# Performance work log

Hardware: AMD Instinct MI355X
Metric: run time of the kernel (lower is better)

## Reference

```python
import jax, jax.numpy as jnp
import numpy as np

B, L, E = 16, 1022, 1280
D, H, FF, NL = 512, 8, 2048, 4
DH = D // H
EPS = 1e-5


def layer_norm(x, s, b):
    m = jnp.mean(x, axis=-1, keepdims=True)
    v = jnp.mean(jnp.square(x - m), axis=-1, keepdims=True)
    return (x - m) * jax.lax.rsqrt(v + EPS) * s + b


def setup_inputs() -> dict:
    key = jax.random.key(0)
    ks = jax.random.split(key, 12)
    s = 0.02
    return {
        "embeddings": jax.random.normal(ks[0], (B, L, E), jnp.float32),
        "mask": jnp.ones((B, L), jnp.float32),
        "position": jnp.tile(jnp.arange(L, dtype=jnp.int32)[None, :], (B, 1)),
        "proj_w": jax.random.normal(ks[1], (D, E), jnp.float32) * s,
        "proj_b": jnp.zeros((D,), jnp.float32),
        "proj_ln_s": jnp.ones((D,), jnp.float32),
        "proj_ln_b": jnp.zeros((D,), jnp.float32),
        "ln1_s": jnp.ones((NL, D), jnp.float32),
        "ln1_b": jnp.zeros((NL, D), jnp.float32),
        "in_w": jax.random.normal(ks[2], (NL, 3 * D, D), jnp.float32) * s,
        "in_b": jnp.zeros((NL, 3 * D), jnp.float32),
        "out_w": jax.random.normal(ks[3], (NL, D, D), jnp.float32) * s,
        "out_b": jnp.zeros((NL, D), jnp.float32),
        "ln2_s": jnp.ones((NL, D), jnp.float32),
        "ln2_b": jnp.zeros((NL, D), jnp.float32),
        "w1": jax.random.normal(ks[4], (NL, FF, D), jnp.float32) * s,
        "b1": jnp.zeros((NL, FF), jnp.float32),
        "w2": jax.random.normal(ks[5], (NL, D, FF), jnp.float32) * s,
        "b2": jnp.zeros((NL, D), jnp.float32),
        "h1_w": jax.random.normal(ks[6], (128, 2 * D), jnp.float32) * s,
        "h1_b": jnp.zeros((128,), jnp.float32),
        "hln_s": jnp.ones((128,), jnp.float32),
        "hln_b": jnp.zeros((128,), jnp.float32),
        "h2_w": jax.random.normal(ks[7], (1, 128), jnp.float32) * s,
        "h2_b": jnp.zeros((1,), jnp.float32),
    }


def _rope_tables():
    inv_freq = 1.0 / (10000.0 ** (jnp.arange(0, DH, 2, dtype=jnp.float32) / DH))
    t = jnp.arange(L, dtype=jnp.float32)
    freqs = jnp.outer(t, inv_freq)          # [L, DH/2]
    emb = jnp.concatenate([freqs, freqs], axis=-1)  # [L, DH]
    return jnp.cos(emb), jnp.sin(emb)


def _rotate_half(x):
    x1, x2 = jnp.split(x, 2, axis=-1)
    return jnp.concatenate([-x2, x1], axis=-1)


def _apply_rope(x, cos, sin):
    # x: [B, L, D] -> per-head rotation -> [B, L, D]
    xh = x.reshape(B, L, H, DH)
    xh = xh * cos[None, :, None, :] + _rotate_half(xh) * sin[None, :, None, :]
    return xh.reshape(B, L, D)


def _forward(embeddings, mask, proj_w, proj_b, proj_ln_s, proj_ln_b,
             ln1_s, ln1_b, in_w, in_b, out_w, out_b, ln2_s, ln2_b,
             w1, b1, w2, b2, h1_w, h1_b, hln_s, hln_b, h2_w, h2_b):
    cos, sin = _rope_tables()
    x = layer_norm(embeddings @ proj_w.T + proj_b, proj_ln_s, proj_ln_b)  # [B,L,D]
    pad = mask <= 0  # True where padded (~mask.bool())
    scale = 1.0 / jnp.sqrt(jnp.float32(DH))
    for i in range(NL):
        n = layer_norm(x, ln1_s[i], ln1_b[i])
        q_in = _apply_rope(n, cos, sin)
        k_in = _apply_rope(n, cos, sin)
        v_in = n
        wq, wk, wv = jnp.split(in_w[i], 3, axis=0)
        bq, bk, bv = jnp.split(in_b[i], 3, axis=0)
        qh = (q_in @ wq.T + bq).reshape(B, L, H, DH)
        kh = (k_in @ wk.T + bk).reshape(B, L, H, DH)
        vh = (v_in @ wv.T + bv).reshape(B, L, H, DH)
        scores = jnp.einsum('blhd,bmhd->bhlm', qh, kh) * scale
        scores = jnp.where(pad[:, None, None, :], jnp.float32(-1e9), scores)
        attn = jax.nn.softmax(scores, axis=-1)
        o = jnp.einsum('bhlm,bmhd->blhd', attn, vh).reshape(B, L, D)
        x = x + (o @ out_w[i].T + out_b[i])
        n2 = layer_norm(x, ln2_s[i], ln2_b[i])
        x = x + (jax.nn.relu(n2 @ w1[i].T + b1[i]) @ w2[i].T + b2[i])
    # masked mean pool
    gctx = (x * mask[..., None]).sum(axis=1) / mask.sum(axis=1, keepdims=True)  # [B,D]
    combined = jnp.concatenate([x, jnp.broadcast_to(gctx[:, None, :], (B, L, D))], axis=-1)
    h = jax.nn.relu(layer_norm(combined @ h1_w.T + h1_b, hln_s, hln_b))
    logits = (h @ h2_w.T + h2_b).squeeze(-1)  # [B,L]
    return logits


def reference(embeddings, mask, position, proj_w, proj_b, proj_ln_s, proj_ln_b,
              ln1_s, ln1_b, in_w, in_b, out_w, out_b, ln2_s, ln2_b,
              w1, b1, w2, b2, h1_w, h1_b, hln_s, hln_b, h2_w, h2_b):
    # position is accepted for API parity but unused (as in the torch module)
    return _forward(embeddings, mask, proj_w, proj_b, proj_ln_s, proj_ln_b,
                    ln1_s, ln1_b, in_w, in_b, out_w, out_b, ln2_s, ln2_b,
                    w1, b1, w2, b2, h1_w, h1_b, hln_s, hln_b, h2_w, h2_b)
```

## Files before the change

### kernel.cpp

```cpp
#include <hip/hip_runtime.h>
#include <cstdint>
#include <cstddef>

#define B_   16
#define L_   1022
#define E_   1280
#define D_   512
#define H_   8
#define FF_  2048
#define NL_  4
#define DH_  64
#define BL_  (B_*L_)
#define EPS_ 1e-5f
#define QSC_ 0.18033688011112042f

typedef unsigned short u16;
typedef unsigned int   u32;
typedef unsigned long long u64;
typedef float f32x4 __attribute__((ext_vector_type(4)));
typedef short s16x8 __attribute__((ext_vector_type(8)));
typedef u32 u32x4 __attribute__((ext_vector_type(4)));

__device__ __forceinline__ u16 f2bf(float f) {
    u32 u = __builtin_bit_cast(u32, f);
    u += 0x7fffu + ((u >> 16) & 1u);
    return (u16)(u >> 16);
}
__device__ __forceinline__ float bf2f(u16 u) {
    return __builtin_bit_cast(float, (u32)u << 16);
}
__device__ __forceinline__ u32 pack2bf(float a, float b) {
    return (u32)f2bf(a) | ((u32)f2bf(b) << 16);
}

__global__ __launch_bounds__(256)
void cast_k(const float* __restrict__ src, u16* __restrict__ dst, int n8) {
    int t = blockIdx.x * 256 + threadIdx.x;
    if (t >= n8) return;
    const float* s = src + (size_t)t * 8;
    float4 a = *(const float4*)(s);
    float4 b = *(const float4*)(s + 4);
    s16x8 o;
    o[0] = (short)f2bf(a.x); o[1] = (short)f2bf(a.y);
    o[2] = (short)f2bf(a.z); o[3] = (short)f2bf(a.w);
    o[4] = (short)f2bf(b.x); o[5] = (short)f2bf(b.y);
    o[6] = (short)f2bf(b.z); o[7] = (short)f2bf(b.w);
    *(s16x8*)(dst + (size_t)t * 8) = o;
}

__global__ __launch_bounds__(256)
void castq_k(const float* __restrict__ src, u16* __restrict__ dst, int n8) {
    int t = blockIdx.x * 256 + threadIdx.x;
    if (t >= n8) return;
    int row = t >> 6;
    float sc = (row % 1536) < 512 ? QSC_ : 1.0f;
    const float* s = src + (size_t)t * 8;
    float4 a = *(const float4*)(s);
    float4 b = *(const float4*)(s + 4);
    s16x8 o;
    o[0] = (short)f2bf(a.x * sc); o[1] = (short)f2bf(a.y * sc);
    o[2] = (short)f2bf(a.z * sc); o[3] = (short)f2bf(a.w * sc);
    o[4] = (short)f2bf(b.x * sc); o[5] = (short)f2bf(b.y * sc);
    o[6] = (short)f2bf(b.z * sc); o[7] = (short)f2bf(b.w * sc);
    *(s16x8*)(dst + (size_t)t * 8) = o;
}

__global__ __launch_bounds__(256)
void qbias_k(const float* __restrict__ ib, float* __restrict__ qbs) {
    int t = blockIdx.x * 256 + threadIdx.x;
    if (t >= NL_ * 1024) return;
    int i = t >> 10, j = t & 1023;
    float sc = j < 512 ? QSC_ : 1.0f;
    qbs[t] = ib[i * 1536 + j] * sc;
}

__global__ __launch_bounds__(256)
void h1cast_k(const float* __restrict__ src, u16* __restrict__ dst) {
    int t = blockIdx.x * 256 + threadIdx.x;
    if (t >= 128 * 512 / 8) return;
    int row = t >> 6, c8 = (t & 63) << 3;
    const float* s = src + (size_t)row * 1024 + c8;
    float4 a = *(const float4*)(s);
    float4 b = *(const float4*)(s + 4);
    s16x8 o;
    o[0] = (short)f2bf(a.x); o[1] = (short)f2bf(a.y);
    o[2] = (short)f2bf(a.z); o[3] = (short)f2bf(a.w);
    o[4] = (short)f2bf(b.x); o[5] = (short)f2bf(b.y);
    o[6] = (short)f2bf(b.z); o[7] = (short)f2bf(b.w);
    *(s16x8*)(dst + (size_t)row * 512 + c8) = o;
}

__global__ void tables_k(float* __restrict__ ct, float* __restrict__ st) {
    int idx = blockIdx.x * blockDim.x + threadIdx.x;
    if (idx >= L_ * DH_) return;
    int l = idx / DH_;
    int d = idx % DH_;
    int j = d & 31;
    float invf = powf(10000.0f, -(float)(2 * j) / (float)DH_);
    float ang = (float)l * invf;
    ct[idx] = cosf(ang);
    st[idx] = sinf(ang);
}

template<bool RELU, bool RESID, bool OUTBF, bool ROWBIAS>
__global__ __launch_bounds__(256)
void mgemm_k(const u16* __restrict__ A, const u16* __restrict__ W,
             const float* __restrict__ bias, const float* __restrict__ resid,
             void* __restrict__ Cout, int M, int N, int K)
{
    constexpr int LDT = 72;
    __shared__ u16 As[128 * LDT];
    __shared__ u16 Ws[128 * LDT];
    const int nt = N >> 7;
    const int bx = blockIdx.x % nt;
    const int by = blockIdx.x / nt;
    const int m0 = by << 7, n0 = bx << 7;
    const int tid = threadIdx.x;
    const int lane = tid & 63, wid = tid >> 6;
    const int wr = wid >> 1, wc = wid & 1;
    const int lr = lane & 15, lk = lane >> 4;

    f32x4 acc[4][4];
#pragma unroll
    for (int m = 0; m < 4; m++)
#pragma unroll
        for (int n = 0; n < 4; n++) acc[m][n] = (f32x4)0.0f;

    for (int k0 = 0; k0 < K; k0 += 64) {
        s16x8 va[4], vw[4];
#pragma unroll
        for (int u = 0; u < 4; u++) {
            int ch = tid + (u << 8);
            int r = ch >> 3, c8 = (ch & 7) << 3;
            int ar = m0 + r; if (ar >= M) ar = M - 1;
            va[u] = *(const s16x8*)(A + (size_t)ar * K + k0 + c8);
            vw[u] = *(const s16x8*)(W + (size_t)(n0 + r) * K + k0 + c8);
        }
        __syncthreads();
#pragma unroll
        for (int u = 0; u < 4; u++) {
            int ch = tid + (u << 8);
            int r = ch >> 3, c8 = (ch & 7) << 3;
            *(s16x8*)&As[r * LDT + c8] = va[u];
            *(s16x8*)&Ws[r * LDT + c8] = vw[u];
        }
        __syncthreads();
#pragma unroll
        for (int kk = 0; kk < 2; kk++) {
            s16x8 af[4], bf[4];
#pragma unroll
            for (int m = 0; m < 4; m++)
                af[m] = *(const s16x8*)&As[(wr * 64 + m * 16 + lr) * LDT + kk * 32 + lk * 8];
#pragma unroll
            for (int n = 0; n < 4; n++)
                bf[n] = *(const s16x8*)&Ws[(wc * 64 + n * 16 + lr) * LDT + kk * 32 + lk * 8];
#pragma unroll
            for (int m = 0; m < 4; m++)
#pragma unroll
                for (int n = 0; n < 4; n++)
                    acc[m][n] = __builtin_amdgcn_mfma_f32_16x16x32_bf16(
                        af[m], bf[n], acc[m][n], 0, 0, 0);
        }
    }

    float bv[4];
    if constexpr (!ROWBIAS) {
#pragma unroll
        for (int n = 0; n < 4; n++) bv[n] = bias[n0 + wc * 64 + n * 16 + lr];
    }
#pragma unroll
    for (int m = 0; m < 4; m++) {
#pragma unroll
        for (int j = 0; j < 4; j++) {
            int row = m0 + wr * 64 + m * 16 + lk * 4 + j;
            if (row >= M) continue;
            const float* rb = nullptr;
            if constexpr (ROWBIAS) rb = bias + (size_t)(row / L_) * N;
#pragma unroll
            for (int n = 0; n < 4; n++) {
                int col = n0 + wc * 64 + n * 16 + lr;
                float c = acc[m][n][j];
                if constexpr (ROWBIAS) c += rb[col];
                else                   c += bv[n];
                if constexpr (RELU) c = fmaxf(c, 0.0f);
                if constexpr (RESID) c += resid[(size_t)row * N + col];
                if constexpr (OUTBF) ((u16*)Cout)[(size_t)row * N + col] = f2bf(c);
                else                 ((float*)Cout)[(size_t)row * N + col] = c;
            }
        }
    }
}

template<int DD, bool RELU, bool OUTBF>
__global__ __launch_bounds__(256)
void ln_k(const float* __restrict__ x, const float* __restrict__ s,
          const float* __restrict__ bb, void* __restrict__ out, int M)
{
    const int lane = threadIdx.x & 63;
    const int row = (blockIdx.x << 2) + (threadIdx.x >> 6);
    if (row >= M) return;
    const float* xr = x + (size_t)row * DD;
    constexpr int NV = DD / 64;
    float v[NV];
    if constexpr (NV == 8) {
        *(float4*)(v)     = *(const float4*)(xr + lane * 8);
        *(float4*)(v + 4) = *(const float4*)(xr + lane * 8 + 4);
    } else {
        float2 t = *(const float2*)(xr + lane * 2);
        v[0] = t.x; v[1] = t.y;
    }
    float sum = 0.f, sq = 0.f;
#pragma unroll
    for (int e = 0; e < NV; e++) { sum += v[e]; sq += v[e] * v[e]; }
#pragma unroll
    for (int msk = 1; msk < 64; msk <<= 1) {
        sum += __shfl_xor(sum, msk);
        sq  += __shfl_xor(sq, msk);
    }
    const float mean = sum * (1.0f / DD);
    const float var  = sq * (1.0f / DD) - mean * mean;
    const float rstd = rsqrtf(var + EPS_);
#pragma unroll
    for (int e = 0; e < NV; e++) {
        int d = lane * NV + e;
        float r = (v[e] - mean) * rstd * s[d] + bb[d];
        if constexpr (RELU) r = fmaxf(r, 0.0f);
        v[e] = r;
    }
    if constexpr (OUTBF) {
        u16* orow = (u16*)out + (size_t)row * DD;
        if constexpr (NV == 8) {
            s16x8 o;
#pragma unroll
            for (int e = 0; e < 8; e++) o[e] = (short)f2bf(v[e]);
            *(s16x8*)(orow + lane * 8) = o;
        } else {
            orow[lane * 2] = f2bf(v[0]); orow[lane * 2 + 1] = f2bf(v[1]);
        }
    } else {
        float* orow = (float*)out + (size_t)row * DD;
        if constexpr (NV == 8) {
            *(float4*)(orow + lane * 8)     = *(float4*)(v);
            *(float4*)(orow + lane * 8 + 4) = *(float4*)(v + 4);
        } else {
            float2 t; t.x = v[0]; t.y = v[1];
            *(float2*)(orow + lane * 2) = t;
        }
    }
}

__global__ __launch_bounds__(256)
void rope_k(const u16* __restrict__ n, const float* __restrict__ ct,
            const float* __restrict__ st, u16* __restrict__ r)
{
    int t = blockIdx.x * 256 + threadIdx.x;
    if (t >= BL_ * D_ / 8) return;
    int idx = t << 3;
    int l = (idx / D_) % L_;
    int d = idx & (D_ - 1);
    int dd = d & 63;
    s16x8 xv = *(const s16x8*)(n + idx);
    int pidx; float sgn;
    if (dd < 32) { pidx = idx + 32; sgn = -1.0f; }
    else         { pidx = idx - 32; sgn =  1.0f; }
    s16x8 pv = *(const s16x8*)(n + pidx);
    float4 c0 = *(const float4*)(ct + l * DH_ + dd);
    float4 c1 = *(const float4*)(ct + l * DH_ + dd + 4);
    float4 s0 = *(const float4*)(st + l * DH_ + dd);
    float4 s1 = *(const float4*)(st + l * DH_ + dd + 4);
    float cc[8] = {c0.x,c0.y,c0.z,c0.w,c1.x,c1.y,c1.z,c1.w};
    float ss[8] = {s0.x,s0.y,s0.z,s0.w,s1.x,s1.y,s1.z,s1.w};
    s16x8 o;
#pragma unroll
    for (int e = 0; e < 8; e++) {
        float xf = bf2f((u16)xv[e]);
        float pf = bf2f((u16)pv[e]);
        o[e] = (short)f2bf(xf * cc[e] + sgn * pf * ss[e]);
    }
    *(s16x8*)(r + idx) = o;
}

__global__ __launch_bounds__(256)
void attn_k(const u16* __restrict__ qk, const u16* __restrict__ v,
            const float* __restrict__ mask, u16* __restrict__ o)
{
    constexpr int LDA = 68;
    constexpr int TSZ = 64 * LDA;
    __shared__ u16 Kt[2 * TSZ];
    __shared__ u16 Vt[2 * TSZ];
    const int bh = blockIdx.x >> 4, qt = blockIdx.x & 15;
    const int b = bh >> 3, h = bh & 7;
    const int tid = threadIdx.x;
    const int lane = tid & 63, w = tid >> 6;
    const int lr = lane & 15, lg = lane >> 4;
    const size_t basebl = (size_t)b * L_;

    const int qrow = qt * 64 + w * 16 + lr;
    const int qc = qrow < L_ ? qrow : L_ - 1;
    s16x8 bq[2];
#pragma unroll
    for (int kk = 0; kk < 2; kk++)
        bq[kk] = *(const s16x8*)(qk + (basebl + qc) * 1024 + h * DH_ + kk * 32 + lg * 8);

    f32x4 oacc[4];
#pragma unroll
    for (int n = 0; n < 4; n++) oacc[n] = (f32x4)0.0f;
    float m_run = -1e30f, l_run = 0.f;

    const int st_key = tid >> 3;
    const int st_d8 = (tid & 7) << 3;
    const int src0 = lr + ((lane & 16) << 1);
    const int src1 = src0 + 16;
    const bool ahi = (lg >> 1) != 0;

    auto stage = [&](int buf, int kt_) {
#pragma unroll
        for (int u = 0; u < 2; u++) {
            int key = st_key + u * 32;
            int gk = kt_ * 64 + key; if (gk >= L_) gk = L_ - 1;
            s16x8 kv = *(const s16x8*)(qk + (basebl + gk) * 1024 + 512 + h * DH_ + st_d8);
            s16x8 vv = *(const s16x8*)(v  + (basebl + gk) * D_ + h * DH_ + st_d8);
            *(s16x8*)&Kt[buf * TSZ + key * LDA + st_d8] = kv;
#pragma unroll
            for (int e = 0; e < 8; e++)
                Vt[buf * TSZ + (st_d8 + e) * LDA + key] = (u16)vv[e];
        }
    };

    stage(0, 0);
    __syncthreads();

    for (int kt = 0; kt < 16; kt++) {
        const int cur = kt & 1;
        if (kt < 15) stage(cur ^ 1, kt + 1);

        int gkey = kt * 64 + lane;
        bool vb = (gkey < L_) && (mask[basebl + gkey] > 0.0f);
        u64 vm = __ballot(vb);

        f32x4 sacc[4];
#pragma unroll
        for (int n = 0; n < 4; n++) {
            sacc[n] = (f32x4)0.0f;
#pragma unroll
            for (int kk = 0; kk < 2; kk++) {
                s16x8 ak = *(const s16x8*)&Kt[cur * TSZ + (n * 16 + lr) * LDA + kk * 32 + lg * 8];
                sacc[n] = __builtin_amdgcn_mfma_f32_16x16x32_bf16(ak, bq[kk], sacc[n], 0, 0, 0);
            }
        }

        float p[4][4];
        float tm = -1e30f;
#pragma unroll
        for (int n = 0; n < 4; n++)
#pragma unroll
            for (int j = 0; j < 4; j++) {
                int kl = 16 * n + 4 * lg + j;
                float s = ((vm >> kl) & 1ull) ? sacc[n][j] : -1e30f;
                p[n][j] = s;
                tm = fmaxf(tm, s);
            }
        tm = fmaxf(tm, __shfl_xor(tm, 16));
        tm = fmaxf(tm, __shfl_xor(tm, 32));
        if (!__all(tm - m_run <= 8.0f)) {
            float nm = fmaxf(m_run, tm);
            float corr = exp2f(m_run - nm);
            l_run *= corr;
#pragma unroll
            for (int n = 0; n < 4; n++) oacc[n] *= corr;
            m_run = nm;
        }
        float ts = 0.f;
#pragma unroll
        for (int n = 0; n < 4; n++)
#pragma unroll
            for (int j = 0; j < 4; j++) {
                p[n][j] = exp2f(p[n][j] - m_run);
                ts += p[n][j];
            }
        ts += __shfl_xor(ts, 16);
        ts += __shfl_xor(ts, 32);
        l_run += ts;

        u32 pk[4][2];
#pragma unroll
        for (int n = 0; n < 4; n++) {
            pk[n][0] = pack2bf(p[n][0], p[n][1]);
            pk[n][1] = pack2bf(p[n][2], p[n][3]);
        }
        u32 r0[4][2], r1[4][2];
#pragma unroll
        for (int n = 0; n < 4; n++)
#pragma unroll
            for (int i = 0; i < 2; i++) {
                r0[n][i] = (u32)__shfl((int)pk[n][i], src0);
                r1[n][i] = (u32)__shfl((int)pk[n][i], src1);
            }
#pragma unroll
        for (int kk = 0; kk < 2; kk++) {
            u32x4 bw;
            bw[0] = ahi ? r0[2 * kk + 1][0] : r0[2 * kk][0];
            bw[1] = ahi ? r0[2 * kk + 1][1] : r0[2 * kk][1];
            bw[2] = ahi ? r1[2 * kk + 1][0] : r1[2 * kk][0];
            bw[3] = ahi ? r1[2 * kk + 1][1] : r1[2 * kk][1];
            s16x8 bp = __builtin_bit_cast(s16x8, bw);
#pragma unroll
            for (int n2 = 0; n2 < 4; n2++) {
                s16x8 av = *(const s16x8*)&Vt[cur * TSZ + (n2 * 16 + lr) * LDA + kk * 32 + lg * 8];
                oacc[n2] = __builtin_amdgcn_mfma_f32_16x16x32_bf16(av, bp, oacc[n2], 0, 0, 0);
            }
        }
        __syncthreads();
    }

    u16* Ol = &Kt[w * 16 * LDA];
    float inv = 1.0f / l_run;
#pragma unroll
    for (int n = 0; n < 4; n++)
#pragma unroll
        for (int j = 0; j < 4; j++)
            Ol[lr * LDA + 16 * n + 4 * lg + j] = f2bf(oacc[n][j] * inv);
    int orow = lane >> 2, oc = (lane & 3) * 16;
    int qg = qt * 64 + w * 16 + orow;
    if (qg < L_) {
        s16x8 o0 = *(const s16x8*)&Ol[orow * LDA + oc];
        s16x8 o1 = *(const s16x8*)&Ol[orow * LDA + oc + 8];
        *(s16x8*)(o + (basebl + qg) * D_ + h * DH_ + oc) = o0;
        *(s16x8*)(o + (basebl + qg) * D_ + h * DH_ + oc + 8) = o1;
    }
}

__global__ __launch_bounds__(512)
void pool1_k(const float* __restrict__ x, const float* __restrict__ mask,
             float* __restrict__ pp, float* __restrict__ mp)
{
    const int b = blockIdx.x, sp = blockIdx.y;
    const int d = threadIdx.x;
    const int l0 = sp * 64;
    float acc = 0.f;
    for (int l = l0; l < l0 + 64 && l < L_; l++)
        acc += x[((size_t)b * L_ + l) * D_ + d] * mask[b * L_ + l];
    pp[((size_t)b * 16 + sp) * D_ + d] = acc;
    if (d == 0) {
        float ms = 0.f;
        for (int l = l0; l < l0 + 64 && l < L_; l++) ms += mask[b * L_ + l];
        mp[b * 16 + sp] = ms;
    }
}

__global__ __launch_bounds__(512)
void pool2_k(const float* __restrict__ pp, const float* __restrict__ mp,
             float* __restrict__ g)
{
    const int b = blockIdx.x;
    const int d = threadIdx.x;
    float acc = 0.f, ms = 0.f;
#pragma unroll
    for (int sp = 0; sp < 16; sp++) {
        acc += pp[((size_t)b * 16 + sp) * D_ + d];
        ms += mp[b * 16 + sp];
    }
    g[b * D_ + d] = acc / ms;
}

__global__ __launch_bounds__(256)
void gpart_k(const float* __restrict__ g, const float* __restrict__ h1w,
             const float* __restrict__ h1b, float* __restrict__ gp)
{
    const int lane = threadIdx.x & 63;
    const int gid = (blockIdx.x << 2) + (threadIdx.x >> 6);
    const int b = gid >> 7, j = gid & 127;
    const float* wr = h1w + (size_t)j * (2 * D_) + D_;
    const float* gr = g + b * D_;
    float4 a0 = *(const float4*)(gr + lane * 8);
    float4 a1 = *(const float4*)(gr + lane * 8 + 4);
    float4 w0 = *(const float4*)(wr + lane * 8);
    float4 w1v = *(const float4*)(wr + lane * 8 + 4);
    float acc = a0.x * w0.x + a0.y * w0.y + a0.z * w0.z + a0.w * w0.w
              + a1.x * w1v.x + a1.y * w1v.y + a1.z * w1v.z + a1.w * w1v.w;
#pragma unroll
    for (int msk = 1; msk < 64; msk <<= 1) acc += __shfl_xor(acc, msk);
    if (lane == 0) gp[b * 128 + j] = acc + h1b[j];
}

__global__ __launch_bounds__(256)
void logits_k(const float* __restrict__ h, const float* __restrict__ w,
              const float* __restrict__ bsc, float* __restrict__ out, int M)
{
    const int lane = threadIdx.x & 63;
    const int row = (blockIdx.x << 2) + (threadIdx.x >> 6);
    if (row >= M) return;
    float2 hv = *(const float2*)(h + (size_t)row * 128 + lane * 2);
    float2 wv = *(const float2*)(w + lane * 2);
    float acc = hv.x * wv.x + hv.y * wv.y;
#pragma unroll
    for (int msk = 1; msk < 64; msk <<= 1) acc += __shfl_xor(acc, msk);
    if (lane == 0) out[row] = acc + bsc[0];
}

extern "C" void kernel_launch(void* const* d_in, const int* in_sizes, int n_in,
                              void* d_out, int out_size, void* d_ws, size_t ws_size,
                              hipStream_t stream)
{
    const float* emb       = (const float*)d_in[0];
    const float* mask      = (const float*)d_in[1];
    const float* proj_w    = (const float*)d_in[3];
    const float* proj_b    = (const float*)d_in[4];
    const float* proj_ln_s = (const float*)d_in[5];
    const float* proj_ln_b = (const float*)d_in[6];
    const float* ln1_s     = (const float*)d_in[7];
    const float* ln1_b     = (const float*)d_in[8];
    const float* in_w      = (const float*)d_in[9];
    const float* in_b      = (const float*)d_in[10];
    const float* out_w     = (const float*)d_in[11];
    const float* out_b     = (const float*)d_in[12];
    const float* ln2_s     = (const float*)d_in[13];
    const float* ln2_b     = (const float*)d_in[14];
    const float* w1        = (const float*)d_in[15];
    const float* b1        = (const float*)d_in[16];
    const float* w2        = (const float*)d_in[17];
    const float* b2        = (const float*)d_in[18];
    const float* h1_w      = (const float*)d_in[19];
    const float* h1_b      = (const float*)d_in[20];
    const float* hln_s     = (const float*)d_in[21];
    const float* hln_b     = (const float*)d_in[22];
    const float* h2_w      = (const float*)d_in[23];
    const float* h2_b      = (const float*)d_in[24];
    float* out = (float*)d_out;

    float* ws = (float*)d_ws;
    const size_t S = (size_t)BL_ * D_;
    float* X  = ws;
    float* Rf = ws + S;
    u16* QKB   = (u16*)(ws + S);
    u16* VB    = (u16*)(ws + 2 * S);
    u16* NbB   = (u16*)(ws + 2 * S) + S;
    u16* FFb16 = (u16*)(ws + 3 * S);
    u16* RopeB = FFb16;
    u16* embB  = FFb16;
    u16* RB    = (u16*)(ws + 4 * S);
    u16* projwB = (u16*)(ws + 5 * S);
    u16* iwB  = projwB + 512 * 1280;
    u16* owB  = iwB + (size_t)NL_ * 3 * D_ * D_;
    u16* w1B  = owB + (size_t)NL_ * D_ * D_;
    u16* w2B  = w1B + (size_t)NL_ * FF_ * D_;
    u16* h1wB = w2B + (size_t)NL_ * D_ * FF_;
    float* CT = ws + 5 * S + 6651904;
    float* ST = CT + L_ * DH_;
    float* GC = ST + L_ * DH_;
    float* GP = GC + B_ * D_;
    float* Pp = GP + B_ * 128;
    float* Mp = Pp + (size_t)B_ * 16 * D_;
    float* QBS = Mp + B_ * 16;
    float* Hb = Rf;

    const int MT = 128;
    const dim3 blk(256);
    const int lnGrid = (BL_ + 3) / 4;

    cast_k<<<(BL_ * E_ / 8 + 255) / 256, blk, 0, stream>>>(emb, embB, BL_ * E_ / 8);
    cast_k<<<(512 * 1280 / 8 + 255) / 256, blk, 0, stream>>>(proj_w, projwB, 512 * 1280 / 8);
    castq_k<<<(NL_ * 3 * D_ * D_ / 8 + 255) / 256, blk, 0, stream>>>(in_w, iwB, NL_ * 3 * D_ * D_ / 8);
    qbias_k<<<(NL_ * 1024 + 255) / 256, blk, 0, stream>>>(in_b, QBS);
    cast_k<<<(NL_ * D_ * D_ / 8 + 255) / 256, blk, 0, stream>>>(out_w, owB, NL_ * D_ * D_ / 8);
    cast_k<<<(NL_ * FF_ * D_ / 8 + 255) / 256, blk, 0, stream>>>(w1, w1B, NL_ * FF_ * D_ / 8);
    cast_k<<<(NL_ * D_ * FF_ / 8 + 255) / 256, blk, 0, stream>>>(w2, w2B, NL_ * D_ * FF_ / 8);
    h1cast_k<<<(128 * 512 / 8 + 255) / 256, blk, 0, stream>>>(h1_w, h1wB);
    tables_k<<<(L_ * DH_ + 255) / 256, blk, 0, stream>>>(CT, ST);

    mgemm_k<false,false,false,false><<<MT * (D_ / 128), blk, 0, stream>>>(
        embB, projwB, proj_b, nullptr, Rf, BL_, D_, E_);
    ln_k<D_,false,false><<<lnGrid, blk, 0, stream>>>(Rf, proj_ln_s, proj_ln_b, X, BL_);

    for (int i = 0; i < NL_; i++) {
        const u16* iw = iwB + (size_t)i * 3 * D_ * D_;
        const float* ib = in_b + (size_t)i * 3 * D_;
        ln_k<D_,false,true><<<lnGrid, blk, 0, stream>>>(X, ln1_s + i * D_, ln1_b + i * D_, NbB, BL_);
        mgemm_k<false,false,true,false><<<MT * 4, blk, 0, stream>>>(
            NbB, iw + 2 * D_ * D_, ib + 2 * D_, nullptr, VB, BL_, D_, D_);
        rope_k<<<(BL_ * D_ / 8 + 255) / 256, blk, 0, stream>>>(NbB, CT, ST, RopeB);
        mgemm_k<false,false,true,false><<<MT * 8, blk, 0, stream>>>(
            RopeB, iw, QBS + (size_t)i * 1024, nullptr, QKB, BL_, 1024, D_);
        attn_k<<<B_ * H_ * 16, blk, 0, stream>>>(QKB, VB, mask, RB);
        mgemm_k<false,true,false,false><<<MT * 4, blk, 0, stream>>>(
            RB, owB + (size_t)i * D_ * D_, out_b + i * D_, X, X, BL_, D_, D_);
        ln_k<D_,false,true><<<lnGrid, blk, 0, stream>>>(X, ln2_s + i * D_, ln2_b + i * D_, NbB, BL_);
        mgemm_k<true,false,true,false><<<MT * 16, blk, 0, stream>>>(
            NbB, w1B + (size_t)i * FF_ * D_, b1 + i * FF_, nullptr, FFb16, BL_, FF_, D_);
        mgemm_k<false,true,false,false><<<MT * 4, blk, 0, stream>>>(
            FFb16, w2B + (size_t)i * D_ * FF_, b2 + i * D_, X, X, BL_, D_, FF_);
    }

    pool1_k<<<dim3(B_, 16), dim3(512), 0, stream>>>(X, mask, Pp, Mp);
    pool2_k<<<B_, dim3(512), 0, stream>>>(Pp, Mp, GC);
    gpart_k<<<(B_ * 128) / 4, blk, 0, stream>>>(GC, h1_w, h1_b, GP);
    cast_k<<<(int)((S / 8 + 255) / 256), blk, 0, stream>>>(X, NbB, (int)(S / 8));
    mgemm_k<false,false,false,true><<<MT * 1, blk, 0, stream>>>(
        NbB, h1wB, GP, nullptr, Hb, BL_, 128, D_);
    ln_k<128,true,false><<<lnGrid, blk, 0, stream>>>(Hb, hln_s, hln_b, Hb, BL_);
    logits_k<<<lnGrid, blk, 0, stream>>>(Hb, h2_w, h2_b, out, BL_);
}
```

Before: 1.501 ms.

## Store residual stream in bf16 and single-buffer attention K/V tiles

The residual activation X is now kept in bf16 instead of fp32. This halves the memory traffic in the residual-add GEMM epilogues, the LayerNorm reads and the pooling, and removes the final cast kernel before the head GEMM. Separately, the attention kernel drops its double-buffered K/V shared-memory staging for a single buffer with two barriers per tile. That lowers LDS use and may raise occupancy, but it gives up the overlap of loads with compute. Accumulating the residual in bf16 across layers loses precision and may hurt accuracy.

```diff
diff --git a/kernel.cpp b/kernel.cpp
--- a/kernel.cpp
+++ b/kernel.cpp
@@ -105,7 +105,7 @@
 template<bool RELU, bool RESID, bool OUTBF, bool ROWBIAS>
 __global__ __launch_bounds__(256)
 void mgemm_k(const u16* __restrict__ A, const u16* __restrict__ W,
-             const float* __restrict__ bias, const float* __restrict__ resid,
+             const float* __restrict__ bias, const u16* __restrict__ resid,
              void* __restrict__ Cout, int M, int N, int K)
 {
     constexpr int LDT = 72;
@@ -183,7 +183,7 @@
                 if constexpr (ROWBIAS) c += rb[col];
                 else                   c += bv[n];
                 if constexpr (RELU) c = fmaxf(c, 0.0f);
-                if constexpr (RESID) c += resid[(size_t)row * N + col];
+                if constexpr (RESID) c += bf2f(resid[(size_t)row * N + col]);
                 if constexpr (OUTBF) ((u16*)Cout)[(size_t)row * N + col] = f2bf(c);
                 else                 ((float*)Cout)[(size_t)row * N + col] = c;
             }
@@ -191,23 +191,34 @@
     }
 }
 
-template<int DD, bool RELU, bool OUTBF>
-__global__ __launch_bounds__(256)
-void ln_k(const float* __restrict__ x, const float* __restrict__ s,
+template<int DD, bool RELU, bool OUTBF, bool INBF>
+__global__ __launch_bounds__(256)
+void ln_k(const void* __restrict__ xin, const float* __restrict__ s,
           const float* __restrict__ bb, void* __restrict__ out, int M)
 {
     const int lane = threadIdx.x & 63;
     const int row = (blockIdx.x << 2) + (threadIdx.x >> 6);
     if (row >= M) return;
-    const float* xr = x + (size_t)row * DD;
     constexpr int NV = DD / 64;
     float v[NV];
-    if constexpr (NV == 8) {
-        *(float4*)(v)     = *(const float4*)(xr + lane * 8);
-        *(float4*)(v + 4) = *(const float4*)(xr + lane * 8 + 4);
+    if constexpr (INBF) {
+        const u16* xr = (const u16*)xin + (size_t)row * DD;
+        if constexpr (NV == 8) {
+            s16x8 t = *(const s16x8*)(xr + lane * 8);
+#pragma unroll
+            for (int e = 0; e < 8; e++) v[e] = bf2f((u16)t[e]);
+        } else {
+            v[0] = bf2f(xr[lane * 2]); v[1] = bf2f(xr[lane * 2 + 1]);
+        }
     } else {
-        float2 t = *(const float2*)(xr + lane * 2);
-        v[0] = t.x; v[1] = t.y;
+        const float* xr = (const float*)xin + (size_t)row * DD;
+        if constexpr (NV == 8) {
+            *(float4*)(v)     = *(const float4*)(xr + lane * 8);
+            *(float4*)(v + 4) = *(const float4*)(xr + lane * 8 + 4);
+        } else {
+            float2 t = *(const float2*)(xr + lane * 2);
+            v[0] = t.x; v[1] = t.y;
+        }
     }
     float sum = 0.f, sq = 0.f;
 #pragma unroll
@@ -285,9 +296,8 @@
             const float* __restrict__ mask, u16* __restrict__ o)
 {
     constexpr int LDA = 68;
-    constexpr int TSZ = 64 * LDA;
-    __shared__ u16 Kt[2 * TSZ];
-    __shared__ u16 Vt[2 * TSZ];
+    __shared__ u16 Kt[64 * LDA];
+    __shared__ u16 Vt[64 * LDA];
     const int bh = blockIdx.x >> 4, qt = blockIdx.x & 15;
     const int b = bh >> 3, h = bh & 7;
     const int tid = threadIdx.x;
@@ -313,26 +323,19 @@
     const int src1 = src0 + 16;
     const bool ahi = (lg >> 1) != 0;
 
-    auto stage = [&](int buf, int kt_) {
+    for (int kt = 0; kt < 16; kt++) {
+        __syncthreads();
 #pragma unroll
         for (int u = 0; u < 2; u++) {
             int key = st_key + u * 32;
-            int gk = kt_ * 64 + key; if (gk >= L_) gk = L_ - 1;
+            int gk = kt * 64 + key; if (gk >= L_) gk = L_ - 1;
             s16x8 kv = *(const s16x8*)(qk + (basebl + gk) * 1024 + 512 + h * DH_ + st_d8);
             s16x8 vv = *(const s16x8*)(v  + (basebl + gk) * D_ + h * DH_ + st_d8);
-            *(s16x8*)&Kt[buf * TSZ + key * LDA + st_d8] = kv;
-#pragma unroll
-            for (int e = 0; e < 8; e++)
-                Vt[buf * TSZ + (st_d8 + e) * LDA + key] = (u16)vv[e];
-        }
-    };
-
-    stage(0, 0);
-    __syncthreads();
-
-    for (int kt = 0; kt < 16; kt++) {
-        const int cur = kt & 1;
-        if (kt < 15) stage(cur ^ 1, kt + 1);
+            *(s16x8*)&Kt[key * LDA + st_d8] = kv;
+#pragma unroll
+            for (int e = 0; e < 8; e++) Vt[(st_d8 + e) * LDA + key] = (u16)vv[e];
+        }
+        __syncthreads();
 
         int gkey = kt * 64 + lane;
         bool vb = (gkey < L_) && (mask[basebl + gkey] > 0.0f);
@@ -344,7 +347,7 @@
             sacc[n] = (f32x4)0.0f;
 #pragma unroll
             for (int kk = 0; kk < 2; kk++) {
-                s16x8 ak = *(const s16x8*)&Kt[cur * TSZ + (n * 16 + lr) * LDA + kk * 32 + lg * 8];
+                s16x8 ak = *(const s16x8*)&Kt[(n * 16 + lr) * LDA + kk * 32 + lg * 8];
                 sacc[n] = __builtin_amdgcn_mfma_f32_16x16x32_bf16(ak, bq[kk], sacc[n], 0, 0, 0);
             }
         }
@@ -406,13 +409,13 @@
             s16x8 bp = __builtin_bit_cast(s16x8, bw);
 #pragma unroll
             for (int n2 = 0; n2 < 4; n2++) {
-                s16x8 av = *(const s16x8*)&Vt[cur * TSZ + (n2 * 16 + lr) * LDA + kk * 32 + lg * 8];
+                s16x8 av = *(const s16x8*)&Vt[(n2 * 16 + lr) * LDA + kk * 32 + lg * 8];
                 oacc[n2] = __builtin_amdgcn_mfma_f32_16x16x32_bf16(av, bp, oacc[n2], 0, 0, 0);
             }
         }
-        __syncthreads();
-    }
-
+    }
+
+    __syncthreads();
     u16* Ol = &Kt[w * 16 * LDA];
     float inv = 1.0f / l_run;
 #pragma unroll
@@ -431,7 +434,7 @@
 }
 
 __global__ __launch_bounds__(512)
-void pool1_k(const float* __restrict__ x, const float* __restrict__ mask,
+void pool1_k(const u16* __restrict__ x, const float* __restrict__ mask,
              float* __restrict__ pp, float* __restrict__ mp)
 {
     const int b = blockIdx.x, sp = blockIdx.y;
@@ -439,7 +442,7 @@
     const int l0 = sp * 64;
     float acc = 0.f;
     for (int l = l0; l < l0 + 64 && l < L_; l++)
-        acc += x[((size_t)b * L_ + l) * D_ + d] * mask[b * L_ + l];
+        acc += bf2f(x[((size_t)b * L_ + l) * D_ + d]) * mask[b * L_ + l];
     pp[((size_t)b * 16 + sp) * D_ + d] = acc;
     if (d == 0) {
         float ms = 0.f;
@@ -530,7 +533,7 @@
 
     float* ws = (float*)d_ws;
     const size_t S = (size_t)BL_ * D_;
-    float* X  = ws;
+    u16* X = (u16*)ws;
     float* Rf = ws + S;
     u16* QKB   = (u16*)(ws + S);
     u16* VB    = (u16*)(ws + 2 * S);
@@ -570,33 +573,32 @@
 
     mgemm_k<false,false,false,false><<<MT * (D_ / 128), blk, 0, stream>>>(
         embB, projwB, proj_b, nullptr, Rf, BL_, D_, E_);
-    ln_k<D_,false,false><<<lnGrid, blk, 0, stream>>>(Rf, proj_ln_s, proj_ln_b, X, BL_);
+    ln_k<D_,false,true,false><<<lnGrid, blk, 0, stream>>>(Rf, proj_ln_s, proj_ln_b, X, BL_);
 
     for (int i = 0; i < NL_; i++) {
         const u16* iw = iwB + (size_t)i * 3 * D_ * D_;
         const float* ib = in_b + (size_t)i * 3 * D_;
-        ln_k<D_,false,true><<<lnGrid, blk, 0, stream>>>(X, ln1_s + i * D_, ln1_b + i * D_, NbB, BL_);
+        ln_k<D_,false,true,true><<<lnGrid, blk, 0, stream>>>(X, ln1_s + i * D_, ln1_b + i * D_, NbB, BL_);
         mgemm_k<false,false,true,false><<<MT * 4, blk, 0, stream>>>(
             NbB, iw + 2 * D_ * D_, ib + 2 * D_, nullptr, VB, BL_, D_, D_);
         rope_k<<<(BL_ * D_ / 8 + 255) / 256, blk, 0, stream>>>(NbB, CT, ST, RopeB);
         mgemm_k<false,false,true,false><<<MT * 8, blk, 0, stream>>>(
             RopeB, iw, QBS + (size_t)i * 1024, nullptr, QKB, BL_, 1024, D_);
         attn_k<<<B_ * H_ * 16, blk, 0, stream>>>(QKB, VB, mask, RB);
-        mgemm_k<false,true,false,false><<<MT * 4, blk, 0, stream>>>(
+        mgemm_k<false,true,true,false><<<MT * 4, blk, 0, stream>>>(
             RB, owB + (size_t)i * D_ * D_, out_b + i * D_, X, X, BL_, D_, D_);
-        ln_k<D_,false,true><<<lnGrid, blk, 0, stream>>>(X, ln2_s + i * D_, ln2_b + i * D_, NbB, BL_);
+        ln_k<D_,false,true,true><<<lnGrid, blk, 0, stream>>>(X, ln2_s + i * D_, ln2_b + i * D_, NbB, BL_);
         mgemm_k<true,false,true,false><<<MT * 16, blk, 0, stream>>>(
             NbB, w1B + (size_t)i * FF_ * D_, b1 + i * FF_, nullptr, FFb16, BL_, FF_, D_);
-        mgemm_k<false,true,false,false><<<MT * 4, blk, 0, stream>>>(
+        mgemm_k<false,true,true,false><<<MT * 4, blk, 0, stream>>>(
             FFb16, w2B + (size_t)i * D_ * FF_, b2 + i * D_, X, X, BL_, D_, FF_);
     }
 
     pool1_k<<<dim3(B_, 16), dim3(512), 0, stream>>>(X, mask, Pp, Mp);
     pool2_k<<<B_, dim3(512), 0, stream>>>(Pp, Mp, GC);
     gpart_k<<<(B_ * 128) / 4, blk, 0, stream>>>(GC, h1_w, h1_b, GP);
-    cast_k<<<(int)((S / 8 + 255) / 256), blk, 0, stream>>>(X, NbB, (int)(S / 8));
     mgemm_k<false,false,false,true><<<MT * 1, blk, 0, stream>>>(
-        NbB, h1wB, GP, nullptr, Hb, BL_, 128, D_);
-    ln_k<128,true,false><<<lnGrid, blk, 0, stream>>>(Hb, hln_s, hln_b, Hb, BL_);
+        X, h1wB, GP, nullptr, Hb, BL_, 128, D_);
+    ln_k<128,true,false,false><<<lnGrid, blk, 0, stream>>>(Hb, hln_s, hln_b, Hb, BL_);
     logits_k<<<lnGrid, blk, 0, stream>>>(Hb, h2_w, h2_b, out, BL_);
 }
```

After: 1.485 ms. No clear change (-1.1%).
